# Optimization experiments

Measured on AMD Instinct MI355X. Metric: run time of the kernel, lower is better.

Reference implementation:

```python
import jax, jax.numpy as jnp
import numpy as np

# SymBranch: delta_i = |h_i - h_pi(i)| (0 if unpaired) -> ResNetMLP -> per-graph
# mean pairwise-L2 scores -> softmax(s/tau) -> weighted sum pooling.
# ResNetMLP (reconstructed, eval mode: dropout=identity):
#   h = x @ W_in + b_in
#   for each block: h = h + relu(LN(h @ Wk + bk))
#   z = LN_out(h @ W_out + b_out)   (last_norm=True)

B, NPG, IN_DIM, HID, EMB, NBLK = 64, 1024, 64, 256, 128, 3
TAU = 0.25
LN_EPS = 1e-5


def _ln(x, g, b):
    mu = jnp.mean(x, axis=-1, keepdims=True)
    var = jnp.var(x, axis=-1, keepdims=True)
    return (x - mu) * jax.lax.rsqrt(var + LN_EPS) * g + b


def setup_inputs() -> dict:
    key = jax.random.key(0)
    ks = jax.random.split(key, 8)
    N = B * NPG
    H = jax.random.normal(ks[0], (N, IN_DIM), jnp.float32)
    batch_ptr = jnp.arange(B + 1, dtype=jnp.int32) * NPG  # equal-size graphs
    # symmetric pairs: node i in first half of each graph paired with i + NPG/2
    half = NPG // 2
    base = (jnp.arange(B, dtype=jnp.int32) * NPG)[:, None]
    li = (base + jnp.arange(half, dtype=jnp.int32)[None, :]).reshape(-1)
    ri = (base + half + jnp.arange(half, dtype=jnp.int32)[None, :]).reshape(-1)
    pairs = jnp.stack([li, ri], axis=1)  # [M,2] global indices
    W_in = jax.random.normal(ks[1], (IN_DIM, HID), jnp.float32) * (1.0 / np.sqrt(IN_DIM))
    b_in = jnp.zeros((HID,), jnp.float32)
    Wb = jax.random.normal(ks[2], (NBLK, HID, HID), jnp.float32) * (1.0 / np.sqrt(HID))
    bb = jnp.zeros((NBLK, HID), jnp.float32)
    lng = jnp.ones((NBLK, HID), jnp.float32)
    lnb = jnp.zeros((NBLK, HID), jnp.float32)
    W_out = jax.random.normal(ks[3], (HID, EMB), jnp.float32) * (1.0 / np.sqrt(HID))
    b_out = jnp.zeros((EMB,), jnp.float32)
    lnf_g = jnp.ones((EMB,), jnp.float32)
    lnf_b = jnp.zeros((EMB,), jnp.float32)
    return dict(H=H, batch_ptr=batch_ptr, pairs=pairs, W_in=W_in, b_in=b_in,
                Wb=Wb, bb=bb, lng=lng, lnb=lnb, W_out=W_out, b_out=b_out,
                lnf_g=lnf_g, lnf_b=lnf_b)


def reference(H, batch_ptr, pairs, W_in, b_in, Wb, bb, lng, lnb, W_out, b_out, lnf_g, lnf_b):
    # gather-diff-scatter: delta_i = |h_i - h_pair(i)|, 0 for unpaired nodes
    li, ri = pairs[:, 0], pairs[:, 1]
    diff = jnp.abs(H[li] - H[ri])                       # [M, in_dim]
    delta = jnp.zeros_like(H).at[li].set(diff).at[ri].set(diff)  # [N, in_dim]
    # ResNetMLP (eval: dropout off)
    h = delta @ W_in + b_in                             # [N, HID]
    for k in range(NBLK):
        h = h + jax.nn.relu(_ln(h @ Wb[k] + bb[k], lng[k], lnb[k]))
    z = _ln(h @ W_out + b_out, lnf_g, lnf_b)            # [N, EMB]
    # per-graph mean pairwise L2 (graphs are equal-sized: reshape is the batched
    # equivalent of the python loop over batch_ptr slices)
    zb = z.reshape(B, NPG, EMB)
    sq = jnp.sum(zb * zb, axis=-1)                      # [B, n]
    d2 = sq[:, :, None] + sq[:, None, :] - 2.0 * jnp.einsum('bne,bme->bnm', zb, zb)
    dist = jnp.sqrt(jnp.clip(d2, 1e-12))                # [B, n, n]
    s = jnp.mean(dist, axis=-1)                         # [B, n]
    w = jax.nn.softmax(s / TAU, axis=-1)                # [B, n]
    f = jnp.einsum('bn,bne->be', w, zb)                 # [B, EMB]
    return f, w
```

## Files before the change

kernel.cpp:

```cpp
#include <hip/hip_runtime.h>
#include <hip/hip_bf16.h>

using bf16 = __hip_bfloat16;
typedef __attribute__((ext_vector_type(8))) short  bfrag;
typedef __attribute__((ext_vector_type(4))) float  ffrag;

#define DEVFN static __device__ __forceinline__

constexpr int BATCH  = 64;
constexpr int NPG    = 1024;
constexpr int IN_DIM = 64;
constexpr int HID    = 256;
constexpr int EMB    = 128;
constexpr int NPAIR  = BATCH * NPG / 2;
constexpr float TAU    = 0.25f;
constexpr float LN_EPS = 1e-5f;

constexpr int MT  = 32;
constexpr int LDH = 264;

DEVFN float b2f(unsigned short u) {
    union { unsigned int i; float f; } x; x.i = ((unsigned int)u) << 16; return x.f;
}
DEVFN unsigned short f2b(float f) {
    bf16 h = __float2bfloat16(f);
    unsigned short u; __builtin_memcpy(&u, &h, 2); return u;
}

__global__ __launch_bounds__(256) void prep_w_kernel(
    const float* __restrict__ Win, const float* __restrict__ Wb,
    const float* __restrict__ Wout,
    unsigned short* __restrict__ WinT, unsigned short* __restrict__ WbT,
    unsigned short* __restrict__ WoutT)
{
    __shared__ short t[64][72];
    const int bid = blockIdx.x, tid = threadIdx.x;
    const float* S; unsigned short* D; int N_, K_, k0, n0;
    if (bid < 48) {
        int mat = bid >> 4, tt = bid & 15;
        S = Wb + mat * 65536; D = WbT + mat * 65536;
        K_ = 256; N_ = 256; k0 = (tt >> 2) * 64; n0 = (tt & 3) * 64;
    } else if (bid < 52) {
        int tt = bid - 48;
        S = Win; D = WinT; K_ = 64; N_ = 256; k0 = 0; n0 = tt * 64;
    } else {
        int tt = bid - 52;
        S = Wout; D = WoutT; K_ = 256; N_ = 128; k0 = (tt >> 1) * 64; n0 = (tt & 1) * 64;
    }
    #pragma unroll
    for (int it = 0; it < 4; ++it) {
        int idx = it * 256 + tid;
        int kk = idx >> 4, n4 = idx & 15;
        float4 v = *(const float4*)(S + (size_t)(k0 + kk) * N_ + n0 + n4 * 4);
        t[n4 * 4 + 0][kk] = (short)f2b(v.x);
        t[n4 * 4 + 1][kk] = (short)f2b(v.y);
        t[n4 * 4 + 2][kk] = (short)f2b(v.z);
        t[n4 * 4 + 3][kk] = (short)f2b(v.w);
    }
    __syncthreads();
    const int KB = K_ >> 5, nb = n0 >> 6;
    #pragma unroll
    for (int it = 0; it < 2; ++it) {
        int u = it * 256 + tid;
        int kbL = u >> 8, rem = u & 255;
        int j = rem >> 6, ln = rem & 63;
        int l16 = ln & 15, qd = ln >> 4;
        bfrag val = *(const bfrag*)&t[j * 16 + l16][kbL * 32 + qd * 8];
        size_t dst = (((size_t)(nb * KB + (k0 >> 5) + kbL) * 4 + j) * 64 + ln) * 8;
        *(bfrag*)(D + dst) = val;
    }
}

template<int K, int N, int MODE>
DEVFN void gemm_phase(short* hbuf, float (*part)[8],
                      const unsigned short* __restrict__ Bf,
                      const float* __restrict__ bias,
                      const float* __restrict__ gamma,
                      const float* __restrict__ beta,
                      unsigned short* __restrict__ Zb,
                      float* __restrict__ sqout, int m0)
{
    constexpr int WN = N / 64;
    constexpr int WM = 4 / WN;
    constexpr int RM = (MT / WM) / 16;
    constexpr int RN = 4;
    constexpr int KB = K / 32;

    const int tid  = threadIdx.x;
    const int wave = tid >> 6, lane = tid & 63;
    const int quad = lane >> 4, l16 = lane & 15;
    const int wrow = (wave / WN) * (MT / WM);
    const int wcol = (wave % WN) * 64;

    __syncthreads();

    ffrag acc[RM][RN];
    #pragma unroll
    for (int i = 0; i < RM; i++)
        #pragma unroll
        for (int j = 0; j < RN; j++)
            #pragma unroll
            for (int r = 0; r < 4; r++) acc[i][j][r] = 0.f;

    const unsigned short* bq = Bf + (size_t)(wcol >> 6) * KB * 2048
                                  + (size_t)lane * 8;

    bfrag b0[RN], b1[RN], b2[RN];
    bfrag acur[RM], anx[RM];
    #pragma unroll
    for (int j = 0; j < RN; j++)
        b0[j] = *(const bfrag*)(bq + j * 512);
    if constexpr (KB > 1) {
        #pragma unroll
        for (int j = 0; j < RN; j++)
            b1[j] = *(const bfrag*)(bq + (4 + j) * 512);
    }
    #pragma unroll
    for (int i = 0; i < RM; i++)
        acur[i] = *(const bfrag*)&hbuf[(wrow + i * 16 + l16) * LDH + quad * 8];

    #pragma unroll
    for (int kb = 0; kb < KB; kb++) {
        if (kb + 2 < KB) {
            #pragma unroll
            for (int j = 0; j < RN; j++)
                b2[j] = *(const bfrag*)(bq + ((kb + 2) * 4 + j) * 512);
        }
        if (kb + 1 < KB) {
            #pragma unroll
            for (int i = 0; i < RM; i++)
                anx[i] = *(const bfrag*)&hbuf[(wrow + i * 16 + l16) * LDH
                                              + (kb + 1) * 32 + quad * 8];
        }
        #pragma unroll
        for (int i = 0; i < RM; i++)
            #pragma unroll
            for (int j = 0; j < RN; j++)
                acc[i][j] = __builtin_amdgcn_mfma_f32_16x16x32_bf16(
                                acur[i], b0[j], acc[i][j], 0, 0, 0);
        if (kb + 1 < KB) {
            #pragma unroll
            for (int j = 0; j < RN; j++) { b0[j] = b1[j]; b1[j] = b2[j]; }
            #pragma unroll
            for (int i = 0; i < RM; i++) acur[i] = anx[i];
        }
    }

    float bia[RN], gam[RN], bet[RN];
    #pragma unroll
    for (int j = 0; j < RN; j++) {
        int gcol = wcol + j * 16 + l16;
        bia[j] = bias[gcol];
        if constexpr (MODE != 0) { gam[j] = gamma[gcol]; bet[j] = beta[gcol]; }
    }
    #pragma unroll
    for (int i = 0; i < RM; i++)
        #pragma unroll
        for (int j = 0; j < RN; j++)
            #pragma unroll
            for (int r = 0; r < 4; r++) acc[i][j][r] += bia[j];

    if constexpr (MODE == 0) {
        __syncthreads();
        #pragma unroll
        for (int i = 0; i < RM; i++)
            #pragma unroll
            for (int j = 0; j < RN; j++) {
                int gcol = wcol + j * 16 + l16;
                #pragma unroll
                for (int r = 0; r < 4; r++) {
                    int row = wrow + i * 16 + quad * 4 + r;
                    hbuf[row * LDH + gcol] = (short)f2b(acc[i][j][r]);
                }
            }
    } else {
        #pragma unroll
        for (int i = 0; i < RM; i++) {
            #pragma unroll
            for (int r = 0; r < 4; r++) {
                float s1 = 0.f, s2 = 0.f;
                #pragma unroll
                for (int j = 0; j < RN; j++) {
                    float x = acc[i][j][r]; s1 += x; s2 += x * x;
                }
                #pragma unroll
                for (int m = 1; m < 16; m <<= 1) {
                    s1 += __shfl_xor(s1, m); s2 += __shfl_xor(s2, m);
                }
                if (l16 == 0) {
                    int row = wrow + i * 16 + quad * 4 + r;
                    part[row][(wave % WN) * 2]     = s1;
                    part[row][(wave % WN) * 2 + 1] = s2;
                }
            }
        }
        __syncthreads();
        float s3a[RM][4];
        #pragma unroll
        for (int i = 0; i < RM; i++) {
            #pragma unroll
            for (int r = 0; r < 4; r++) {
                int row = wrow + i * 16 + quad * 4 + r;
                float s1 = 0.f, s2 = 0.f;
                #pragma unroll
                for (int wn = 0; wn < WN; wn++) {
                    s1 += part[row][wn * 2]; s2 += part[row][wn * 2 + 1];
                }
                float mean = s1 * (1.f / N);
                float rstd = rsqrtf(s2 * (1.f / N) - mean * mean + LN_EPS);
                float s3 = 0.f;
                #pragma unroll
                for (int j = 0; j < RN; j++) {
                    int gcol = wcol + j * 16 + l16;
                    float y = (acc[i][j][r] - mean) * rstd * gam[j] + bet[j];
                    if constexpr (MODE == 1) {
                        float res = b2f((unsigned short)hbuf[row * LDH + gcol]);
                        y = fmaxf(y, 0.f) + res;
                        hbuf[row * LDH + gcol] = (short)f2b(y);
                    } else {
                        unsigned short ub = f2b(y);
                        Zb[(size_t)(m0 + row) * EMB + gcol] = ub;
                        float yr = b2f(ub);
                        s3 += yr * yr;
                    }
                }
                s3a[i][r] = s3;
            }
        }
        if constexpr (MODE == 2) {
            __syncthreads();
            #pragma unroll
            for (int i = 0; i < RM; i++)
                #pragma unroll
                for (int r = 0; r < 4; r++) {
                    float s3 = s3a[i][r];
                    #pragma unroll
                    for (int m = 1; m < 16; m <<= 1) s3 += __shfl_xor(s3, m);
                    if (l16 == 0) {
                        int row = wrow + i * 16 + quad * 4 + r;
                        part[row][wave % WN] = s3;
                    }
                }
            __syncthreads();
            if (l16 == 0 && (wave % WN) == 0) {
                #pragma unroll
                for (int i = 0; i < RM; i++)
                    #pragma unroll
                    for (int r = 0; r < 4; r++) {
                        int row = wrow + i * 16 + quad * 4 + r;
                        float t = 0.f;
                        #pragma unroll
                        for (int wn = 0; wn < WN; wn++) t += part[row][wn];
                        sqout[m0 + row] = t;
                    }
            }
        }
    }
}

__global__ __launch_bounds__(256, 3) void fused_mlp_kernel(
    const float* __restrict__ H, const int* __restrict__ pairs,
    const unsigned short* __restrict__ WinT,
    const unsigned short* __restrict__ WbT,
    const unsigned short* __restrict__ WoutT,
    const float* __restrict__ b_in,  const float* __restrict__ bb,
    const float* __restrict__ lng,   const float* __restrict__ lnb,
    const float* __restrict__ b_out, const float* __restrict__ lnf_g,
    const float* __restrict__ lnf_b,
    unsigned short* __restrict__ Zb, float* __restrict__ sq)
{
    __shared__ __align__(16) short hbuf[MT * LDH];
    __shared__ float part[MT][8];

    const int tid = threadIdx.x;
    const int m0  = blockIdx.x * MT;

    #pragma unroll
    for (int it = 0; it < 2; ++it) {
        int idx = tid + it * 256;
        int r = idx >> 4, c4 = idx & 15;
        int p = m0 + r;
        int li = pairs[2 * p], ri = pairs[2 * p + 1];
        float4 a = *(const float4*)(H + (size_t)li * IN_DIM + c4 * 4);
        float4 b = *(const float4*)(H + (size_t)ri * IN_DIM + c4 * 4);
        short4 s;
        s.x = (short)f2b(fabsf(a.x - b.x));
        s.y = (short)f2b(fabsf(a.y - b.y));
        s.z = (short)f2b(fabsf(a.z - b.z));
        s.w = (short)f2b(fabsf(a.w - b.w));
        *(short4*)&hbuf[r * LDH + c4 * 4] = s;
    }

    gemm_phase<IN_DIM, HID, 0>(hbuf, part, WinT, b_in,
                               nullptr, nullptr, nullptr, nullptr, m0);
    gemm_phase<HID, HID, 1>(hbuf, part, WbT,
                            bb,       lng,       lnb,       nullptr, nullptr, m0);
    gemm_phase<HID, HID, 1>(hbuf, part, WbT + 65536,
                            bb + 256, lng + 256, lnb + 256, nullptr, nullptr, m0);
    gemm_phase<HID, HID, 1>(hbuf, part, WbT + 131072,
                            bb + 512, lng + 512, lnb + 512, nullptr, nullptr, m0);
    gemm_phase<HID, EMB, 2>(hbuf, part, WoutT, b_out,
                            lnf_g, lnf_b, Zb, sq, m0);
}

__global__ __launch_bounds__(256) void gram_kernel(
    const unsigned short* __restrict__ Z, const float* __restrict__ sq,
    float* __restrict__ srowP)
{
    constexpr int LDU = EMB + 8;
    __shared__ __align__(16) short Brows[2][64 * LDU];

    const int batch = blockIdx.x >> 4;
    const int rt    = (blockIdx.x >> 1) & 7;
    const int hf    = blockIdx.x & 1;
    const int tid = threadIdx.x, wave = tid >> 6, lane = tid & 63;
    const int quad = lane >> 4, l16 = lane & 15;
    const int urow0 = batch * 512;
    const int ar0   = urow0 + rt * 64;
    const int arow  = ar0 + wave * 16 + l16;

    bfrag a4[4];
    #pragma unroll
    for (int kk = 0; kk < 4; kk++)
        a4[kk] = *(const bfrag*)(Z + (size_t)arow * EMB + kk * 32 + quad * 8);

    float rs[4] = {0.f, 0.f, 0.f, 0.f};
    float sqr[4];
    #pragma unroll
    for (int r = 0; r < 4; r++)
        sqr[r] = sq[ar0 + wave * 16 + quad * 4 + r];

    const int sr = tid >> 4, sc = (tid & 15) * 8;
    bfrag g[4];
    #pragma unroll
    for (int it = 0; it < 4; ++it)
        g[it] = *(const bfrag*)(Z + (size_t)(urow0 + hf * 256 + it * 16 + sr) * EMB + sc);

    for (int c = 0; c < 4; ++c) {
        const int cur = c & 1;
        #pragma unroll
        for (int it = 0; it < 4; ++it)
            *(bfrag*)&Brows[cur][(it * 16 + sr) * LDU + sc] = g[it];
        if (c < 3) {
            #pragma unroll
            for (int it = 0; it < 4; ++it)
                g[it] = *(const bfrag*)(Z + (size_t)(urow0 + hf * 256 + (c + 1) * 64
                                                     + it * 16 + sr) * EMB + sc);
        }
        __syncthreads();
        int ch = hf * 4 + c;
        ffrag acc[4];
        #pragma unroll
        for (int j = 0; j < 4; j++)
            #pragma unroll
            for (int r = 0; r < 4; r++) acc[j][r] = 0.f;
        #pragma unroll
        for (int kk = 0; kk < 4; ++kk)
            #pragma unroll
            for (int j = 0; j < 4; j++) {
                bfrag b = *(const bfrag*)&Brows[cur][(j * 16 + l16) * LDU
                                                     + kk * 32 + quad * 8];
                acc[j] = __builtin_amdgcn_mfma_f32_16x16x32_bf16(a4[kk], b,
                                                                 acc[j], 0, 0, 0);
            }
        #pragma unroll
        for (int j = 0; j < 4; j++) {
            float sqc = sq[urow0 + ch * 64 + j * 16 + l16];
            #pragma unroll
            for (int r = 0; r < 4; r++) {
                float d2 = sqr[r] + sqc - 2.f * acc[j][r];
                rs[r] += sqrtf(fmaxf(d2, 1e-12f));
            }
        }
    }
    #pragma unroll
    for (int r = 0; r < 4; r++) {
        float v = rs[r];
        v += __shfl_xor(v, 1); v += __shfl_xor(v, 2);
        v += __shfl_xor(v, 4); v += __shfl_xor(v, 8);
        if (l16 == 0)
            srowP[hf * (BATCH * 512) + batch * 512 + rt * 64
                  + wave * 16 + quad * 4 + r] = v;
    }
}

__global__ __launch_bounds__(1024) void softmax_f_kernel(
    const float* __restrict__ srowP, const unsigned short* __restrict__ Z,
    float* __restrict__ fout, float* __restrict__ wout)
{
    const int b = blockIdx.x, tid = threadIdx.x;
    __shared__ float wsh[512];
    __shared__ float red[16];
    __shared__ float fred[8][128];
    constexpr float SC = (1.f / 512.f) * (1.f / TAU);

    const int wv = tid >> 6, lane = tid & 63;
    float l0 = 0.f, e0 = 0.f;
    if (tid < 512) {
        l0 = (srowP[b * 512 + tid] + srowP[BATCH * 512 + b * 512 + tid]) * SC;
        float mx = l0;
        #pragma unroll
        for (int m = 1; m < 64; m <<= 1) mx = fmaxf(mx, __shfl_xor(mx, m));
        if (lane == 0) red[wv] = mx;
    }
    __syncthreads();
    float mx = red[0];
    #pragma unroll
    for (int i = 1; i < 8; i++) mx = fmaxf(mx, red[i]);
    if (tid < 512) {
        e0 = expf(l0 - mx);
        float s = e0;
        #pragma unroll
        for (int m = 1; m < 64; m <<= 1) s += __shfl_xor(s, m);
        if (lane == 0) red[8 + wv] = s;
    }
    __syncthreads();
    float sum = 0.f;
    #pragma unroll
    for (int i = 0; i < 8; i++) sum += red[8 + i];
    float inv = 1.f / sum;
    if (tid < 512) wsh[tid] = e0 * inv;
    __syncthreads();
    wout[b * 1024 + tid] = wsh[tid & 511] * 0.5f;

    const int g = tid >> 7, e = tid & 127;
    const unsigned short* zp = Z + (size_t)(b * 512 + g * 64) * EMB + e;
    float acc = 0.f;
    #pragma unroll 8
    for (int c = 0; c < 64; c++)
        acc += wsh[g * 64 + c] * b2f(zp[(size_t)c * EMB]);
    fred[g][e] = acc;
    __syncthreads();
    if (tid < 128) {
        float t = 0.f;
        #pragma unroll
        for (int gg = 0; gg < 8; gg++) t += fred[gg][e];
        fout[b * EMB + e] = t;
    }
}

extern "C" void kernel_launch(void* const* d_in, const int* in_sizes, int n_in,
                              void* d_out, int out_size, void* d_ws, size_t ws_size,
                              hipStream_t stream)
{
    (void)in_sizes; (void)n_in; (void)out_size; (void)ws_size;
    const float* H     = (const float*)d_in[0];
    const int*   pairs = (const int*)d_in[2];
    const float* W_in  = (const float*)d_in[3];
    const float* b_in  = (const float*)d_in[4];
    const float* Wb    = (const float*)d_in[5];
    const float* bb    = (const float*)d_in[6];
    const float* lng   = (const float*)d_in[7];
    const float* lnb   = (const float*)d_in[8];
    const float* W_out = (const float*)d_in[9];
    const float* b_out = (const float*)d_in[10];
    const float* lnf_g = (const float*)d_in[11];
    const float* lnf_b = (const float*)d_in[12];

    float* f_out = (float*)d_out;
    float* w_out = (float*)d_out + BATCH * EMB;

    char* ws = (char*)d_ws;
    size_t off = 0;
    auto carve = [&](size_t bytes) -> void* {
        void* p = ws + off;
        off += (bytes + 255) & ~(size_t)255;
        return p;
    };
    unsigned short* WinT  = (unsigned short*)carve((size_t)HID * IN_DIM * 2);
    unsigned short* WbT   = (unsigned short*)carve((size_t)3 * HID * HID * 2);
    unsigned short* WoutT = (unsigned short*)carve((size_t)EMB * HID * 2);
    unsigned short* Zb    = (unsigned short*)carve((size_t)NPAIR * EMB * 2);
    float*          sq    = (float*)carve((size_t)NPAIR * 4);
    float*          srowP = (float*)carve((size_t)2 * BATCH * 512 * 4);

    prep_w_kernel<<<60, 256, 0, stream>>>(W_in, Wb, W_out, WinT, WbT, WoutT);

    fused_mlp_kernel<<<NPAIR / MT, 256, 0, stream>>>(
        H, pairs, WinT, WbT, WoutT,
        b_in, bb, lng, lnb, b_out, lnf_g, lnf_b, Zb, sq);

    gram_kernel<<<BATCH * 16, 256, 0, stream>>>(Zb, sq, srowP);
    softmax_f_kernel<<<BATCH, 1024, 0, stream>>>(srowP, Zb, f_out, w_out);
}
```

Measured before the change: 142.5 us.

## Switch GEMM prefetch to double buffering, cap occupancy at two blocks via LDS padding

```diff
diff --git a/kernel.cpp b/kernel.cpp
--- a/kernel.cpp
+++ b/kernel.cpp
@@ -18,6 +18,7 @@
 
 constexpr int MT  = 32;
 constexpr int LDH = 264;
+constexpr int HPAD = 11520;
 
 DEVFN float b2f(unsigned short u) {
     union { unsigned int i; float f; } x; x.i = ((unsigned int)u) << 16; return x.f;
@@ -105,45 +106,32 @@
     const unsigned short* bq = Bf + (size_t)(wcol >> 6) * KB * 2048
                                   + (size_t)lane * 8;
 
-    bfrag b0[RN], b1[RN], b2[RN];
-    bfrag acur[RM], anx[RM];
+    bfrag Ab[2][RM], Bb[2][RN];
     #pragma unroll
     for (int j = 0; j < RN; j++)
-        b0[j] = *(const bfrag*)(bq + j * 512);
-    if constexpr (KB > 1) {
-        #pragma unroll
-        for (int j = 0; j < RN; j++)
-            b1[j] = *(const bfrag*)(bq + (4 + j) * 512);
-    }
+        Bb[0][j] = *(const bfrag*)(bq + j * 512);
     #pragma unroll
     for (int i = 0; i < RM; i++)
-        acur[i] = *(const bfrag*)&hbuf[(wrow + i * 16 + l16) * LDH + quad * 8];
+        Ab[0][i] = *(const bfrag*)&hbuf[(wrow + i * 16 + l16) * LDH + quad * 8];
 
     #pragma unroll
     for (int kb = 0; kb < KB; kb++) {
-        if (kb + 2 < KB) {
+        const int cur = kb & 1, nxt = cur ^ 1;
+        if (kb + 1 < KB) {
             #pragma unroll
             for (int j = 0; j < RN; j++)
-                b2[j] = *(const bfrag*)(bq + ((kb + 2) * 4 + j) * 512);
-        }
-        if (kb + 1 < KB) {
+                Bb[nxt][j] = *(const bfrag*)(bq + ((kb + 1) * 4 + j) * 512);
             #pragma unroll
             for (int i = 0; i < RM; i++)
-                anx[i] = *(const bfrag*)&hbuf[(wrow + i * 16 + l16) * LDH
-                                              + (kb + 1) * 32 + quad * 8];
+                Ab[nxt][i] = *(const bfrag*)&hbuf[(wrow + i * 16 + l16) * LDH
+                                                  + (kb + 1) * 32 + quad * 8];
         }
         #pragma unroll
         for (int i = 0; i < RM; i++)
             #pragma unroll
             for (int j = 0; j < RN; j++)
                 acc[i][j] = __builtin_amdgcn_mfma_f32_16x16x32_bf16(
-                                acur[i], b0[j], acc[i][j], 0, 0, 0);
-        if (kb + 1 < KB) {
-            #pragma unroll
-            for (int j = 0; j < RN; j++) { b0[j] = b1[j]; b1[j] = b2[j]; }
-            #pragma unroll
-            for (int i = 0; i < RM; i++) acur[i] = anx[i];
-        }
+                                Ab[cur][i], Bb[cur][j], acc[i][j], 0, 0, 0);
     }
 
     float bia[RN], gam[RN], bet[RN];
@@ -258,7 +246,7 @@
     }
 }
 
-__global__ __launch_bounds__(256, 3) void fused_mlp_kernel(
+__global__ __launch_bounds__(256, 2) void fused_mlp_kernel(
     const float* __restrict__ H, const int* __restrict__ pairs,
     const unsigned short* __restrict__ WinT,
     const unsigned short* __restrict__ WbT,
@@ -269,7 +257,7 @@
     const float* __restrict__ lnf_b,
     unsigned short* __restrict__ Zb, float* __restrict__ sq)
 {
-    __shared__ __align__(16) short hbuf[MT * LDH];
+    __shared__ __align__(16) short hbuf[MT * LDH + HPAD];
     __shared__ float part[MT][8];
 
     const int tid = threadIdx.x;
```

After: 141.6 us. About the same (-0.6%).
